# Performance work log

Measured on AMD Instinct MI355X. Metric: run time of the kernel, lower is better.

The kernel has to match this reference:

```python
import jax, jax.numpy as jnp
import numpy as np

N = 4096          # nproteins
IN_F = 512        # in_features
OUT_F = 64        # out_features
ALPHA = 0.2       # leakyrelu slope
EPS = 1e-5        # batchnorm eps
NEG = -9e15       # mask fill value from the original code


def setup_inputs() -> dict:
    key = jax.random.key(0)
    k = jax.random.split(key, 5)
    h = jax.random.normal(k[0], (N, IN_F), dtype=jnp.float32)
    # sparse 0/1 adjacency (avg degree ~20) stored dense, as the module expects
    adj = (jax.random.uniform(k[1], (N, N)) < 0.005).astype(jnp.float32)
    half = IN_F // 2
    # xavier_uniform with gain=1.414 ~ U(-b, b), b = gain*sqrt(6/(fan_in+fan_out))
    b_w = 1.414 * np.sqrt(6.0 / (half + OUT_F))
    W1 = jax.random.uniform(k[2], (half, OUT_F), minval=-b_w, maxval=b_w, dtype=jnp.float32)
    W2 = jax.random.uniform(k[3], (half, OUT_F), minval=-b_w, maxval=b_w, dtype=jnp.float32)
    b_a = 1.414 * np.sqrt(6.0 / (2 * OUT_F + 1))
    a = jax.random.uniform(k[4], (2 * OUT_F, 1), minval=-b_a, maxval=b_a, dtype=jnp.float32)
    gamma = jnp.ones((2 * OUT_F,), dtype=jnp.float32)   # bn2 weight
    beta = jnp.zeros((2 * OUT_F,), dtype=jnp.float32)   # bn2 bias
    return {"h": h, "adj": adj, "W1": W1, "W2": W2, "a": a, "gamma": gamma, "beta": beta}


def _lrelu(x):
    return jnp.where(x > 0, x, ALPHA * x)


def reference(h, adj, W1, W2, a, gamma, beta):
    d = h.shape[1] // 2
    Wh1 = h[:, :d] @ W1          # [N, F]
    Wh2 = h[:, d:] @ W2          # [N, F]

    def prep(Wh):
        s1 = Wh @ a[:OUT_F]      # [N, 1]
        s2 = Wh @ a[OUT_F:]      # [N, 1]
        return _lrelu(s1 + s2.T)  # [N, N]

    e1 = prep(Wh1)
    e2 = prep(Wh2)

    adj2 = adj @ adj                               # 2-hop counts [N, N]
    adj2 = adj2 - jnp.diag(jnp.diag(adj2))         # zero the diagonal

    att1 = jax.nn.softmax(jnp.where(adj > 0, e1, NEG), axis=1)
    h_prime1 = att1 @ Wh1                          # [N, F]
    att2 = jax.nn.softmax(jnp.where(adj2 > 0, e2, NEG), axis=1)
    h_prime2 = att2 @ Wh2                          # [N, F]

    hp = jnp.concatenate([h_prime1, h_prime2], axis=-1)  # [N, 2F]
    # BatchNorm1d (training-mode batch stats, biased variance)
    mean = hp.mean(axis=0)
    var = hp.var(axis=0)
    out = gamma * (hp - mean) / jnp.sqrt(var + EPS) + beta
    return _lrelu(out)  # concat=True branch
```

## Files before the change

### kernel.cpp

```cpp
#include <hip/hip_runtime.h>
#include <hip/hip_bf16.h>

#define NN 4096
#define IN_F 512
#define HALF 256
#define FF 64
#define ALPHA 0.2f
#define EPSV 1e-5f
#define CAP2 1024

typedef unsigned long long u64;
typedef unsigned int u32;

__device__ __forceinline__ float lrelu(float x){ return x > 0.f ? x : ALPHA * x; }

__global__ __launch_bounds__(256) void pack_kernel(const float* __restrict__ adj,
                                                   u64* __restrict__ packA) {
    int i = blockIdx.x;
    int tid = threadIdx.x;
    int wave = tid >> 6, lane = tid & 63;
    const float* row = adj + (size_t)i * NN;
    #pragma unroll
    for (int t = 0; t < NN / 256; ++t) {
        int col = t * 256 + tid;
        u64 m = __ballot(row[col] > 0.f);
        if (lane == 0) packA[(size_t)i * 64 + t * 4 + wave] = m;
    }
}

__global__ __launch_bounds__(128) void wh_kernel(const float* __restrict__ h,
                                                 const float* __restrict__ W1,
                                                 const float* __restrict__ W2,
                                                 const float* __restrict__ a,
                                                 float* __restrict__ Wh1,
                                                 float* __restrict__ Wh2,
                                                 float* __restrict__ s11,
                                                 float* __restrict__ s12,
                                                 float* __restrict__ s21,
                                                 float* __restrict__ s22) {
    __shared__ float hs[4 * IN_F];
    int r0 = blockIdx.x * 4;
    int tid = threadIdx.x;
    const float4* hsrc = (const float4*)(h + (size_t)r0 * IN_F);
    float4* hdst = (float4*)hs;
    #pragma unroll
    for (int t = 0; t < 4; ++t) hdst[tid + 128 * t] = hsrc[tid + 128 * t];
    __syncthreads();

    int wave = tid >> 6, f = tid & 63;
    const float* W = wave ? W2 : W1;
    const float* hw = hs + wave * HALF;
    float acc0 = 0.f, acc1 = 0.f, acc2 = 0.f, acc3 = 0.f;
    #pragma unroll 4
    for (int k = 0; k < HALF; ++k) {
        float w = W[k * FF + f];
        acc0 += hw[k] * w;
        acc1 += hw[IN_F + k] * w;
        acc2 += hw[2 * IN_F + k] * w;
        acc3 += hw[3 * IN_F + k] * w;
    }
    float* Wh = wave ? Wh2 : Wh1;
    Wh[(size_t)(r0 + 0) * FF + f] = acc0;
    Wh[(size_t)(r0 + 1) * FF + f] = acc1;
    Wh[(size_t)(r0 + 2) * FF + f] = acc2;
    Wh[(size_t)(r0 + 3) * FF + f] = acc3;

    float a1 = a[f], a2 = a[64 + f];
    #pragma unroll
    for (int r = 0; r < 4; ++r) {
        float acc = (r == 0) ? acc0 : (r == 1) ? acc1 : (r == 2) ? acc2 : acc3;
        float v1 = acc * a1, v2 = acc * a2;
        #pragma unroll
        for (int off = 32; off; off >>= 1) {
            v1 += __shfl_down(v1, off, 64);
            v2 += __shfl_down(v2, off, 64);
        }
        if (f == 0) {
            if (wave == 0) { s11[r0 + r] = v1; s12[r0 + r] = v2; }
            else           { s21[r0 + r] = v1; s22[r0 + r] = v2; }
        }
    }
}

__device__ __forceinline__ void softmax_gather(int cnt, const int* __restrict__ nbr,
                                               float* __restrict__ ev,
                                               const float* __restrict__ Wh,
                                               float* __restrict__ outp,
                                               int tid, float* red, float* partial) {
    int wave = tid >> 6, lane = tid & 63;
    float Z;
    if (cnt > 0) {
        float m = -3.4e38f;
        for (int n = tid; n < cnt; n += 256) m = fmaxf(m, ev[n]);
        #pragma unroll
        for (int off = 32; off; off >>= 1) m = fmaxf(m, __shfl_down(m, off, 64));
        if (lane == 0) red[wave] = m;
        __syncthreads();
        m = fmaxf(fmaxf(red[0], red[1]), fmaxf(red[2], red[3]));
        float s = 0.f;
        for (int n = tid; n < cnt; n += 256) {
            float p = __expf(ev[n] - m);
            ev[n] = p;
            s += p;
        }
        #pragma unroll
        for (int off = 32; off; off >>= 1) s += __shfl_down(s, off, 64);
        __syncthreads();
        if (lane == 0) red[wave] = s;
        __syncthreads();
        Z = red[0] + red[1] + red[2] + red[3];
    } else {
        Z = (float)NN;
    }
    int g = tid >> 4;
    int fq = (tid & 15) << 2;
    float ax = 0.f, ay = 0.f, az = 0.f, aw = 0.f;
    if (cnt > 0) {
        for (int n = g; n < cnt; n += 16) {
            float w = ev[n];
            const float4 v = *reinterpret_cast<const float4*>(&Wh[(size_t)nbr[n] * FF + fq]);
            ax += w * v.x; ay += w * v.y; az += w * v.z; aw += w * v.w;
        }
    } else {
        for (int n = g; n < NN; n += 16) {
            const float4 v = *reinterpret_cast<const float4*>(&Wh[(size_t)n * FF + fq]);
            ax += v.x; ay += v.y; az += v.z; aw += v.w;
        }
    }
    float4 accv = make_float4(ax, ay, az, aw);
    *reinterpret_cast<float4*>(&partial[tid << 2]) = accv;
    __syncthreads();
    if (tid < 64) {
        float s = 0.f;
        #pragma unroll
        for (int g2 = 0; g2 < 16; ++g2) s += partial[g2 * 64 + tid];
        outp[tid] = s / Z;
    }
}

__device__ __forceinline__ void build_list(u64 bits, int lane, int* __restrict__ nbr,
                                           float* __restrict__ ev, float si,
                                           const float* __restrict__ sj, int* pcnt) {
    int pc = __popcll(bits);
    int scan = pc;
    #pragma unroll
    for (int off = 1; off < 64; off <<= 1) {
        int v = __shfl_up(scan, off, 64);
        if (lane >= off) scan += v;
    }
    int pos = scan - pc;
    while (bits) {
        int b = __builtin_ctzll(bits);
        bits &= bits - 1;
        int j = (lane << 6) | b;
        if (pos < CAP2) {
            nbr[pos] = j;
            if (sj) ev[pos] = lrelu(si + sj[j]);
        }
        ++pos;
    }
    if (lane == 63) *pcnt = scan;
}

__global__ __launch_bounds__(256) void attn_kernel(const u64* __restrict__ packA,
                                                   const float* __restrict__ Wh1,
                                                   const float* __restrict__ Wh2,
                                                   const float* __restrict__ s11,
                                                   const float* __restrict__ s12,
                                                   const float* __restrict__ s21,
                                                   const float* __restrict__ s22,
                                                   float* __restrict__ hp) {
    __shared__ int   nbr[CAP2];
    __shared__ float ev[CAP2];
    __shared__ u64   maskw[4 * 64];
    __shared__ float red[4];
    __shared__ float partial[1024];
    __shared__ int   scnt;

    int bid = blockIdx.x;
    int tid = threadIdx.x;
    int wave = tid >> 6, lane = tid & 63;
    bool hop2 = bid >= NN;
    int i = hop2 ? bid - NN : bid;

    if (!hop2) {
        if (wave == 0)
            build_list(packA[(size_t)i * 64 + lane], lane, nbr, ev, s11[i], s12, &scnt);
        __syncthreads();
        int c1 = min(scnt, CAP2);
        softmax_gather(c1, nbr, ev, Wh1, hp + (size_t)i * 128, tid, red, partial);
    } else {
        if (wave == 0)
            build_list(packA[(size_t)i * 64 + lane], lane, nbr, ev, 0.f, nullptr, &scnt);
        __syncthreads();
        int c1 = min(scnt, CAP2);
        u64 m = 0;
        for (int n = wave; n < c1; n += 4)
            m |= packA[(size_t)nbr[n] * 64 + lane];
        maskw[wave * 64 + lane] = m;
        __syncthreads();
        if (wave == 0) {
            u64 word = maskw[lane] | maskw[64 + lane] | maskw[128 + lane] | maskw[192 + lane];
            if (lane == (i >> 6)) word &= ~(1ull << (i & 63));
            build_list(word, lane, nbr, ev, s21[i], s22, &scnt);
        }
        __syncthreads();
        int c2 = min(scnt, CAP2);
        softmax_gather(c2, nbr, ev, Wh2, hp + (size_t)i * 128 + 64, tid, red, partial);
    }
}

__global__ __launch_bounds__(256) void stats_kernel(const float* __restrict__ hp,
                                                    float* __restrict__ colsum,
                                                    float* __restrict__ colsq) {
    __shared__ float ls[128], lq[128];
    int tid = threadIdx.x;
    if (tid < 128) { ls[tid] = 0.f; lq[tid] = 0.f; }
    __syncthreads();
    float s0 = 0, s1 = 0, s2 = 0, s3 = 0, q0 = 0, q1 = 0, q2 = 0, q3 = 0;
    const float4* hp4 = (const float4*)hp;
    for (size_t idx = (size_t)blockIdx.x * 256 + tid; idx < (size_t)NN * 32;
         idx += (size_t)gridDim.x * 256) {
        float4 v = hp4[idx];
        s0 += v.x; q0 += v.x * v.x;
        s1 += v.y; q1 += v.y * v.y;
        s2 += v.z; q2 += v.z * v.z;
        s3 += v.w; q3 += v.w * v.w;
    }
    int cb = (tid & 31) << 2;
    atomicAdd(&ls[cb + 0], s0); atomicAdd(&lq[cb + 0], q0);
    atomicAdd(&ls[cb + 1], s1); atomicAdd(&lq[cb + 1], q1);
    atomicAdd(&ls[cb + 2], s2); atomicAdd(&lq[cb + 2], q2);
    atomicAdd(&ls[cb + 3], s3); atomicAdd(&lq[cb + 3], q3);
    __syncthreads();
    if (tid < 128) {
        atomicAdd(&colsum[tid], ls[tid]);
        atomicAdd(&colsq[tid], lq[tid]);
    }
}

__global__ __launch_bounds__(256) void norm_kernel(float* __restrict__ hp,
                                                   const float* __restrict__ colsum,
                                                   const float* __restrict__ colsq,
                                                   const float* __restrict__ gamma,
                                                   const float* __restrict__ beta) {
    size_t idx = (size_t)blockIdx.x * 256 + threadIdx.x;
    if (idx >= (size_t)NN * 32) return;
    int cb = (int)((idx << 2) & 127);
    float4 v = ((const float4*)hp)[idx];
    float r[4] = {v.x, v.y, v.z, v.w};
    #pragma unroll
    for (int t = 0; t < 4; ++t) {
        int c = cb + t;
        float mean = colsum[c] * (1.f / NN);
        float var = colsq[c] * (1.f / NN) - mean * mean;
        float inv = rsqrtf(var + EPSV);
        r[t] = lrelu((r[t] - mean) * inv * gamma[c] + beta[c]);
    }
    ((float4*)hp)[idx] = make_float4(r[0], r[1], r[2], r[3]);
}

extern "C" void kernel_launch(void* const* d_in, const int* in_sizes, int n_in,
                              void* d_out, int out_size, void* d_ws, size_t ws_size,
                              hipStream_t stream) {
    const float* h     = (const float*)d_in[0];
    const float* adj   = (const float*)d_in[1];
    const float* W1    = (const float*)d_in[2];
    const float* W2    = (const float*)d_in[3];
    const float* a     = (const float*)d_in[4];
    const float* gamma = (const float*)d_in[5];
    const float* beta  = (const float*)d_in[6];
    float* hp = (float*)d_out;

    u64* packA  = (u64*)d_ws;
    float* Wh1  = (float*)(packA + (size_t)NN * 64);
    float* Wh2  = Wh1 + (size_t)NN * FF;
    float* s11  = Wh2 + (size_t)NN * FF;
    float* s12  = s11 + NN;
    float* s21  = s12 + NN;
    float* s22  = s21 + NN;
    float* colsum = s22 + NN;
    float* colsq  = colsum + 128;

    hipMemsetAsync(colsum, 0, 256 * sizeof(float), stream);

    pack_kernel<<<NN, 256, 0, stream>>>(adj, packA);
    wh_kernel<<<NN / 4, 128, 0, stream>>>(h, W1, W2, a, Wh1, Wh2, s11, s12, s21, s22);
    attn_kernel<<<2 * NN, 256, 0, stream>>>(packA, Wh1, Wh2, s11, s12, s21, s22, hp);
    stats_kernel<<<256, 256, 0, stream>>>(hp, colsum, colsq);
    norm_kernel<<<(NN * 32 + 255) / 256, 256, 0, stream>>>(hp, colsum, colsq, gamma, beta);
}
```

Before: 189.8 us.

## Process 1-hop attention rows one per wave and drop atomics for column stats

The 1-hop attention path now gives each wave its own row, so 1024 blocks handle four rows each instead of 4096 blocks each using a whole block on about 20 neighbours. The 1-hop lists are capped at 256 entries per wave. The e-value computation moves out of list building into the softmax loop, and reductions use xor shuffles. Column statistics are written as per-block partials and summed by a new single-block finalize kernel, which removes the global atomics and the memset but adds one more launch.

```diff
diff --git a/kernel.cpp b/kernel.cpp
--- a/kernel.cpp
+++ b/kernel.cpp
@@ -8,11 +8,42 @@
 #define ALPHA 0.2f
 #define EPSV 1e-5f
 #define CAP2 1024
+#define H1B 1024
 
 typedef unsigned long long u64;
 typedef unsigned int u32;
 
 __device__ __forceinline__ float lrelu(float x){ return x > 0.f ? x : ALPHA * x; }
+
+__device__ __forceinline__ float wave_fmax(float v){
+    #pragma unroll
+    for (int off = 32; off; off >>= 1) v = fmaxf(v, __shfl_xor(v, off, 64));
+    return v;
+}
+__device__ __forceinline__ float wave_fsum(float v){
+    #pragma unroll
+    for (int off = 32; off; off >>= 1) v += __shfl_xor(v, off, 64);
+    return v;
+}
+
+__device__ __forceinline__ int build_idx(u64 bits, int lane, int cap, int* __restrict__ nbr){
+    int pc = __popcll(bits);
+    int scan = pc;
+    #pragma unroll
+    for (int off = 1; off < 64; off <<= 1) {
+        int v = __shfl_up(scan, off, 64);
+        if (lane >= off) scan += v;
+    }
+    int total = __shfl(scan, 63, 64);
+    int pos = scan - pc;
+    while (bits) {
+        int b = __builtin_ctzll(bits);
+        bits &= bits - 1;
+        if (pos < cap) nbr[pos] = (lane << 6) | b;
+        ++pos;
+    }
+    return total;
+}
 
 __global__ __launch_bounds__(256) void pack_kernel(const float* __restrict__ adj,
                                                    u64* __restrict__ packA) {
@@ -82,86 +113,6 @@
     }
 }
 
-__device__ __forceinline__ void softmax_gather(int cnt, const int* __restrict__ nbr,
-                                               float* __restrict__ ev,
-                                               const float* __restrict__ Wh,
-                                               float* __restrict__ outp,
-                                               int tid, float* red, float* partial) {
-    int wave = tid >> 6, lane = tid & 63;
-    float Z;
-    if (cnt > 0) {
-        float m = -3.4e38f;
-        for (int n = tid; n < cnt; n += 256) m = fmaxf(m, ev[n]);
-        #pragma unroll
-        for (int off = 32; off; off >>= 1) m = fmaxf(m, __shfl_down(m, off, 64));
-        if (lane == 0) red[wave] = m;
-        __syncthreads();
-        m = fmaxf(fmaxf(red[0], red[1]), fmaxf(red[2], red[3]));
-        float s = 0.f;
-        for (int n = tid; n < cnt; n += 256) {
-            float p = __expf(ev[n] - m);
-            ev[n] = p;
-            s += p;
-        }
-        #pragma unroll
-        for (int off = 32; off; off >>= 1) s += __shfl_down(s, off, 64);
-        __syncthreads();
-        if (lane == 0) red[wave] = s;
-        __syncthreads();
-        Z = red[0] + red[1] + red[2] + red[3];
-    } else {
-        Z = (float)NN;
-    }
-    int g = tid >> 4;
-    int fq = (tid & 15) << 2;
-    float ax = 0.f, ay = 0.f, az = 0.f, aw = 0.f;
-    if (cnt > 0) {
-        for (int n = g; n < cnt; n += 16) {
-            float w = ev[n];
-            const float4 v = *reinterpret_cast<const float4*>(&Wh[(size_t)nbr[n] * FF + fq]);
-            ax += w * v.x; ay += w * v.y; az += w * v.z; aw += w * v.w;
-        }
-    } else {
-        for (int n = g; n < NN; n += 16) {
-            const float4 v = *reinterpret_cast<const float4*>(&Wh[(size_t)n * FF + fq]);
-            ax += v.x; ay += v.y; az += v.z; aw += v.w;
-        }
-    }
-    float4 accv = make_float4(ax, ay, az, aw);
-    *reinterpret_cast<float4*>(&partial[tid << 2]) = accv;
-    __syncthreads();
-    if (tid < 64) {
-        float s = 0.f;
-        #pragma unroll
-        for (int g2 = 0; g2 < 16; ++g2) s += partial[g2 * 64 + tid];
-        outp[tid] = s / Z;
-    }
-}
-
-__device__ __forceinline__ void build_list(u64 bits, int lane, int* __restrict__ nbr,
-                                           float* __restrict__ ev, float si,
-                                           const float* __restrict__ sj, int* pcnt) {
-    int pc = __popcll(bits);
-    int scan = pc;
-    #pragma unroll
-    for (int off = 1; off < 64; off <<= 1) {
-        int v = __shfl_up(scan, off, 64);
-        if (lane >= off) scan += v;
-    }
-    int pos = scan - pc;
-    while (bits) {
-        int b = __builtin_ctzll(bits);
-        bits &= bits - 1;
-        int j = (lane << 6) | b;
-        if (pos < CAP2) {
-            nbr[pos] = j;
-            if (sj) ev[pos] = lrelu(si + sj[j]);
-        }
-        ++pos;
-    }
-    if (lane == 63) *pcnt = scan;
-}
-
 __global__ __launch_bounds__(256) void attn_kernel(const u64* __restrict__ packA,
                                                    const float* __restrict__ Wh1,
                                                    const float* __restrict__ Wh2,
@@ -172,47 +123,148 @@
                                                    float* __restrict__ hp) {
     __shared__ int   nbr[CAP2];
     __shared__ float ev[CAP2];
-    __shared__ u64   maskw[4 * 64];
-    __shared__ float red[4];
+    __shared__ u64   maskw[256];
+    __shared__ float red[8];
     __shared__ float partial[1024];
     __shared__ int   scnt;
 
     int bid = blockIdx.x;
     int tid = threadIdx.x;
-    int wave = tid >> 6, lane = tid & 63;
-    bool hop2 = bid >= NN;
-    int i = hop2 ? bid - NN : bid;
-
-    if (!hop2) {
-        if (wave == 0)
-            build_list(packA[(size_t)i * 64 + lane], lane, nbr, ev, s11[i], s12, &scnt);
+    int w = tid >> 6, lane = tid & 63;
+
+    if (bid < H1B) {
+        int row = bid * 4 + w;
+        int*   mynbr  = nbr + w * 256;
+        float* myev   = ev + w * 256;
+        float* mypart = partial + w * 256;
+
+        int total = build_idx(packA[(size_t)row * 64 + lane], lane, 256, mynbr);
+        int c = min(total, 256);
+        __syncthreads();
+
+        float Z;
+        if (c > 0) {
+            float s11i = s11[row];
+            float lm = -3.4e38f;
+            for (int n = lane; n < c; n += 64) {
+                float e = lrelu(s11i + s12[mynbr[n]]);
+                myev[n] = e;
+                lm = fmaxf(lm, e);
+            }
+            float m = wave_fmax(lm);
+            float ls = 0.f;
+            for (int n = lane; n < c; n += 64) {
+                float p = __expf(myev[n] - m);
+                myev[n] = p;
+                ls += p;
+            }
+            Z = wave_fsum(ls);
+        } else {
+            Z = (float)NN;
+        }
+        __syncthreads();
+
+        int g = lane >> 4, fq = (lane & 15) << 2;
+        float ax = 0.f, ay = 0.f, az = 0.f, aw = 0.f;
+        if (c > 0) {
+            #pragma unroll 4
+            for (int n = g; n < c; n += 4) {
+                float wg = myev[n];
+                const float4 v = *reinterpret_cast<const float4*>(&Wh1[(size_t)mynbr[n] * FF + fq]);
+                ax += wg * v.x; ay += wg * v.y; az += wg * v.z; aw += wg * v.w;
+            }
+        } else {
+            #pragma unroll 4
+            for (int n = g; n < NN; n += 4) {
+                const float4 v = *reinterpret_cast<const float4*>(&Wh1[(size_t)n * FF + fq]);
+                ax += v.x; ay += v.y; az += v.z; aw += v.w;
+            }
+        }
+        *reinterpret_cast<float4*>(&mypart[g * 64 + fq]) = make_float4(ax, ay, az, aw);
+        __syncthreads();
+        float s = mypart[lane] + mypart[64 + lane] + mypart[128 + lane] + mypart[192 + lane];
+        hp[(size_t)row * 128 + lane] = s / Z;
+    } else {
+        int i = bid - H1B;
+        if (w == 0) {
+            int t1 = build_idx(packA[(size_t)i * 64 + lane], lane, CAP2, nbr);
+            if (lane == 0) scnt = t1;
+        }
         __syncthreads();
         int c1 = min(scnt, CAP2);
-        softmax_gather(c1, nbr, ev, Wh1, hp + (size_t)i * 128, tid, red, partial);
-    } else {
-        if (wave == 0)
-            build_list(packA[(size_t)i * 64 + lane], lane, nbr, ev, 0.f, nullptr, &scnt);
-        __syncthreads();
-        int c1 = min(scnt, CAP2);
+
         u64 m = 0;
-        for (int n = wave; n < c1; n += 4)
+        for (int n = w; n < c1; n += 4)
             m |= packA[(size_t)nbr[n] * 64 + lane];
-        maskw[wave * 64 + lane] = m;
-        __syncthreads();
-        if (wave == 0) {
+        maskw[w * 64 + lane] = m;
+        __syncthreads();
+
+        if (w == 0) {
             u64 word = maskw[lane] | maskw[64 + lane] | maskw[128 + lane] | maskw[192 + lane];
             if (lane == (i >> 6)) word &= ~(1ull << (i & 63));
-            build_list(word, lane, nbr, ev, s21[i], s22, &scnt);
+            int t2 = build_idx(word, lane, CAP2, nbr);
+            if (lane == 0) scnt = t2;
         }
         __syncthreads();
         int c2 = min(scnt, CAP2);
-        softmax_gather(c2, nbr, ev, Wh2, hp + (size_t)i * 128 + 64, tid, red, partial);
+
+        float Z;
+        if (c2 > 0) {
+            float s21i = s21[i];
+            float lm = -3.4e38f;
+            for (int n = tid; n < c2; n += 256) {
+                float e = lrelu(s21i + s22[nbr[n]]);
+                ev[n] = e;
+                lm = fmaxf(lm, e);
+            }
+            lm = wave_fmax(lm);
+            if (lane == 0) red[w] = lm;
+            __syncthreads();
+            float mx = fmaxf(fmaxf(red[0], red[1]), fmaxf(red[2], red[3]));
+            float ls = 0.f;
+            for (int n = tid; n < c2; n += 256) {
+                float p = __expf(ev[n] - mx);
+                ev[n] = p;
+                ls += p;
+            }
+            ls = wave_fsum(ls);
+            if (lane == 0) red[4 + w] = ls;
+            __syncthreads();
+            Z = red[4] + red[5] + red[6] + red[7];
+        } else {
+            Z = (float)NN;
+        }
+
+        int g = tid >> 4, fq = (tid & 15) << 2;
+        float ax = 0.f, ay = 0.f, az = 0.f, aw = 0.f;
+        if (c2 > 0) {
+            #pragma unroll 4
+            for (int n = g; n < c2; n += 16) {
+                float wg = ev[n];
+                const float4 v = *reinterpret_cast<const float4*>(&Wh2[(size_t)nbr[n] * FF + fq]);
+                ax += wg * v.x; ay += wg * v.y; az += wg * v.z; aw += wg * v.w;
+            }
+        } else {
+            #pragma unroll 4
+            for (int n = g; n < NN; n += 16) {
+                const float4 v = *reinterpret_cast<const float4*>(&Wh2[(size_t)n * FF + fq]);
+                ax += v.x; ay += v.y; az += v.z; aw += v.w;
+            }
+        }
+        *reinterpret_cast<float4*>(&partial[tid << 2]) = make_float4(ax, ay, az, aw);
+        __syncthreads();
+        if (tid < 64) {
+            float s = 0.f;
+            #pragma unroll
+            for (int g2 = 0; g2 < 16; ++g2) s += partial[g2 * 64 + tid];
+            hp[(size_t)i * 128 + 64 + tid] = s / Z;
+        }
     }
 }
 
 __global__ __launch_bounds__(256) void stats_kernel(const float* __restrict__ hp,
-                                                    float* __restrict__ colsum,
-                                                    float* __restrict__ colsq) {
+                                                    float* __restrict__ ps,
+                                                    float* __restrict__ pq) {
     __shared__ float ls[128], lq[128];
     int tid = threadIdx.x;
     if (tid < 128) { ls[tid] = 0.f; lq[tid] = 0.f; }
@@ -234,9 +286,23 @@
     atomicAdd(&ls[cb + 3], s3); atomicAdd(&lq[cb + 3], q3);
     __syncthreads();
     if (tid < 128) {
-        atomicAdd(&colsum[tid], ls[tid]);
-        atomicAdd(&colsq[tid], lq[tid]);
-    }
+        ps[(size_t)blockIdx.x * 128 + tid] = ls[tid];
+        pq[(size_t)blockIdx.x * 128 + tid] = lq[tid];
+    }
+}
+
+__global__ __launch_bounds__(256) void finalize_kernel(const float* __restrict__ ps,
+                                                       const float* __restrict__ pq,
+                                                       float* __restrict__ colsum,
+                                                       float* __restrict__ colsq) {
+    int tid = threadIdx.x;
+    const float* src = (tid < 128) ? ps : pq;
+    int c = tid & 127;
+    float s = 0.f;
+    #pragma unroll 8
+    for (int b = 0; b < 256; ++b) s += src[(size_t)b * 128 + c];
+    if (tid < 128) colsum[c] = s;
+    else           colsq[c]  = s;
 }
 
 __global__ __launch_bounds__(256) void norm_kernel(float* __restrict__ hp,
@@ -279,14 +345,15 @@
     float* s12  = s11 + NN;
     float* s21  = s12 + NN;
     float* s22  = s21 + NN;
-    float* colsum = s22 + NN;
+    float* ps   = s22 + NN;
+    float* pq   = ps + 256 * 128;
+    float* colsum = pq + 256 * 128;
     float* colsq  = colsum + 128;
-
-    hipMemsetAsync(colsum, 0, 256 * sizeof(float), stream);
 
     pack_kernel<<<NN, 256, 0, stream>>>(adj, packA);
     wh_kernel<<<NN / 4, 128, 0, stream>>>(h, W1, W2, a, Wh1, Wh2, s11, s12, s21, s22);
-    attn_kernel<<<2 * NN, 256, 0, stream>>>(packA, Wh1, Wh2, s11, s12, s21, s22, hp);
-    stats_kernel<<<256, 256, 0, stream>>>(hp, colsum, colsq);
+    attn_kernel<<<H1B + NN, 256, 0, stream>>>(packA, Wh1, Wh2, s11, s12, s21, s22, hp);
+    stats_kernel<<<256, 256, 0, stream>>>(hp, ps, pq);
+    finalize_kernel<<<1, 256, 0, stream>>>(ps, pq, colsum, colsq);
     norm_kernel<<<(NN * 32 + 255) / 256, 256, 0, stream>>>(hp, colsum, colsq, gamma, beta);
 }
```

New measurement: 191.2 us. About the same (+0.8%).
